# Performance work log

Measured on AMD Instinct MI355X. Metric: run time of the kernel, lower is better.

The kernel has to match this reference:

```python
import jax, jax.numpy as jnp
import numpy as np

N = 50000
E = 800000
F_IN = 500
H = 5          # heads
C = 32         # per-head channels
HID = H * C    # 160
NC = 20        # num_classes
G = 8          # number of graphs in batch
SLOPE_ATT = 0.2   # GATConv attention leaky slope (PyG default)
SLOPE_ACT = 0.01  # F.leaky_relu default


def _layernorm(x, scale, bias, eps=1e-5):
    mu = jnp.mean(x, axis=-1, keepdims=True)
    var = jnp.var(x, axis=-1, keepdims=True)
    return (x - mu) * jax.lax.rsqrt(var + eps) * scale + bias


def _edge_softmax(logits, dst, num_nodes):
    # segment softmax over incoming edges of each destination node
    m = jax.ops.segment_max(logits, dst, num_segments=num_nodes)
    ex = jnp.exp(logits - m[dst])
    s = jax.ops.segment_sum(ex, dst, num_segments=num_nodes)
    return ex / (s[dst] + 1e-16)


def _gat_layer(x, src, dst, W, a_src, a_dst, b):
    n = x.shape[0]
    h = (x @ W).reshape(n, H, C)                       # [N,H,C]
    al_s = jnp.einsum('nhc,hc->nh', h, a_src)          # [N,H]
    al_d = jnp.einsum('nhc,hc->nh', h, a_dst)
    logits = jax.nn.leaky_relu(al_s[src] + al_d[dst], SLOPE_ATT)  # [Et,H]
    alpha = _edge_softmax(logits, dst, n)              # [Et,H]
    msg = h[src] * alpha[..., None]                    # [Et,H,C]
    out = jax.ops.segment_sum(msg, dst, num_segments=n).reshape(n, HID) + b
    return out, alpha


def setup_inputs():
    key = jax.random.key(0)
    ks = jax.random.split(key, 24)
    p = lambda k, shp: jax.random.normal(k, shp, jnp.float32) * 0.05
    x = jax.random.normal(ks[0], (N, F_IN), jnp.float32)
    edge_index = jax.random.randint(ks[1], (2, E), 0, N, jnp.int64)
    batch = jnp.sort(jax.random.randint(ks[2], (N,), 0, G, jnp.int64))
    return {
        'x': x, 'edge_index': edge_index, 'batch': batch,
        'W1': p(ks[3], (F_IN, HID)), 'a_src1': p(ks[4], (H, C)), 'a_dst1': p(ks[5], (H, C)), 'b1': jnp.zeros((HID,), jnp.float32),
        'ln1_s': jnp.ones((HID,), jnp.float32), 'ln1_b': jnp.zeros((HID,), jnp.float32),
        'W2': p(ks[6], (HID, HID)), 'a_src2': p(ks[7], (H, C)), 'a_dst2': p(ks[8], (H, C)), 'b2': jnp.zeros((HID,), jnp.float32),
        'ln2_s': jnp.ones((HID,), jnp.float32), 'ln2_b': jnp.zeros((HID,), jnp.float32),
        'Wm': p(ks[9], (HID, HID)), 'bm': jnp.zeros((HID,), jnp.float32),
        'Wmlp1': p(ks[10], (HID, HID)), 'bmlp1': jnp.zeros((HID,), jnp.float32),
        'ln3_s': jnp.ones((HID,), jnp.float32), 'ln3_b': jnp.zeros((HID,), jnp.float32),
        'Wmlp2': p(ks[11], (HID, NC)), 'bmlp2': jnp.zeros((NC,), jnp.float32),
    }


def reference(x, edge_index, batch, W1, a_src1, a_dst1, b1, ln1_s, ln1_b,
              W2, a_src2, a_dst2, b2, ln2_s, ln2_b, Wm, bm,
              Wmlp1, bmlp1, ln3_s, ln3_b, Wmlp2, bmlp2):
    n = x.shape[0]
    # PyG GATConv adds self-loops by default
    loops = jnp.arange(n, dtype=edge_index.dtype)
    src = jnp.concatenate([edge_index[0], loops])
    dst = jnp.concatenate([edge_index[1], loops])

    h1, alpha1 = _gat_layer(x, src, dst, W1, a_src1, a_dst1, b1)
    h1 = jax.nn.leaky_relu(h1, SLOPE_ACT)
    h1 = _layernorm(h1, ln1_s, ln1_b)      # dropout = identity at eval

    h2, alpha2 = _gat_layer(h1, src, dst, W2, a_src2, a_dst2, b2)
    h2 = jax.nn.leaky_relu(h2, SLOPE_ACT)
    h2 = _layernorm(h2, ln2_s, ln2_b)

    xo = jax.nn.leaky_relu(h2 @ Wm + bm, SLOPE_ACT)   # [N,HID]

    # global_mean_pool over batch assignment
    sums = jax.ops.segment_sum(xo, batch, num_segments=G)
    cnts = jax.ops.segment_sum(jnp.ones((n, 1), xo.dtype), batch, num_segments=G)
    pooled = sums / jnp.maximum(cnts, 1.0)            # [G,HID]

    z = pooled @ Wmlp1 + bmlp1
    z = jax.nn.relu(_layernorm(z, ln3_s, ln3_b))
    rec = z @ Wmlp2 + bmlp2                           # [G,NC]
    return xo, rec, alpha1, alpha2
```

## Files before the change

### kernel.cpp

```cpp
#include <hip/hip_runtime.h>
#include <hip/hip_bf16.h>
#include <cstdint>
#include <cstddef>

#define NN   50000
#define EE   800000
#define ET_  (EE + NN)
#define FIN  500
#define HID_ 160
#define NC_  20
#define GG   8
#define GB1  ((NN + 63) / 64)
#define NK1  16
#define NK2  5

typedef __attribute__((ext_vector_type(8))) short ab8;
typedef __attribute__((ext_vector_type(4))) float f4;

static __device__ __forceinline__ unsigned short f2bf(float v) {
    union { float f; uint32_t u; } c; c.f = v;
    uint32_t r = c.u + 0x7FFFu + ((c.u >> 16) & 1u);
    return (unsigned short)(r >> 16);
}

static __device__ __forceinline__ float2 bf2f2(uint32_t u) {
    union { uint32_t u; float f; } a, b;
    a.u = u << 16;
    b.u = u & 0xffff0000u;
    return make_float2(a.f, b.f);
}

static __device__ __forceinline__ int lbound_i(const int* arr, int n, int val) {
    int lo = 0, hi = n;
    while (lo < hi) { int mid = (lo + hi) >> 1; if (arr[mid] < val) lo = mid + 1; else hi = mid; }
    return lo;
}

__global__ __launch_bounds__(256) void k_hist(const int* __restrict__ ei, int* __restrict__ deg) {
    int e = blockIdx.x * 256 + threadIdx.x;
    if (e >= ET_) return;
    int d = (e < EE) ? ei[EE + e] : (e - EE);
    atomicAdd(&deg[d], 1);
}

__global__ __launch_bounds__(256) void k_scan1(const int* __restrict__ deg, int* __restrict__ rowptr,
                                               int* __restrict__ bsum) {
    __shared__ int s[256];
    int t = threadIdx.x;
    int base = blockIdx.x * 1024 + t * 4;
    int v0 = (base + 0 < NN) ? deg[base + 0] : 0;
    int v1 = (base + 1 < NN) ? deg[base + 1] : 0;
    int v2 = (base + 2 < NN) ? deg[base + 2] : 0;
    int v3 = (base + 3 < NN) ? deg[base + 3] : 0;
    int tot = v0 + v1 + v2 + v3;
    s[t] = tot;
    __syncthreads();
    for (int off = 1; off < 256; off <<= 1) {
        int y = (t >= off) ? s[t - off] : 0;
        __syncthreads();
        s[t] += y;
        __syncthreads();
    }
    int excl = s[t] - tot;
    if (t == 255) bsum[blockIdx.x] = s[255];
    if (base + 0 < NN) rowptr[base + 0] = excl;  excl += v0;
    if (base + 1 < NN) rowptr[base + 1] = excl;  excl += v1;
    if (base + 2 < NN) rowptr[base + 2] = excl;  excl += v2;
    if (base + 3 < NN) rowptr[base + 3] = excl;
}

__global__ void k_scan2(int* __restrict__ bsum, int nb) {
    int t = threadIdx.x;
    int v = (t < nb) ? bsum[t] : 0;
    int orig = v;
    for (int off = 1; off < 64; off <<= 1) {
        int y = __shfl_up(v, off);
        if (t >= off) v += y;
    }
    if (t < nb) bsum[t] = v - orig;
}

__global__ __launch_bounds__(256) void k_scan3(int* __restrict__ rowptr, const int* __restrict__ bsum,
                                               int* __restrict__ cursor) {
    int i = blockIdx.x * 256 + threadIdx.x;
    if (i < NN) {
        int r = rowptr[i] + bsum[i >> 10];
        rowptr[i] = r;
        cursor[i] = r;
    }
    if (i == NN) rowptr[NN] = ET_;
}

__global__ __launch_bounds__(256) void k_scatter(const int* __restrict__ ei, int* __restrict__ cursor,
                                                 int2* __restrict__ epair) {
    int e = blockIdx.x * 256 + threadIdx.x;
    if (e >= ET_) return;
    int s, d;
    if (e < EE) { s = ei[e]; d = ei[EE + e]; } else { s = e - EE; d = e - EE; }
    int slot = atomicAdd(&cursor[d], 1);
    epair[slot] = make_int2(e, s);
}

__global__ __launch_bounds__(256) void k_prep_all(const float* __restrict__ W1, ab8* __restrict__ B1,
                                                  const float* __restrict__ W2, ab8* __restrict__ B2,
                                                  const float* __restrict__ Wm, ab8* __restrict__ Bm,
                                                  float* __restrict__ pooled) {
    int idx = blockIdx.x * 256 + threadIdx.x;
    if (idx < GG * HID_) pooled[idx] = 0.f;
    const int C1 = NK1 * 10 * 64;
    const int C2 = NK2 * 10 * 64;
    const float* W; ab8* Bo; int K, cidx;
    if (idx < C1)                { W = W1; Bo = B1; K = FIN;  cidx = idx; }
    else if (idx < C1 + C2)      { W = W2; Bo = B2; K = HID_; cidx = idx - C1; }
    else if (idx < C1 + 2 * C2)  { W = Wm; Bo = Bm; K = HID_; cidx = idx - C1 - C2; }
    else return;
    int s = cidx / 640, r = cidx % 640;
    int t = r >> 6, l = r & 63;
    int fr = l & 15, q = l >> 4;
    int n  = t * 16 + fr;
    int k0 = s * 32 + q * 8;
    unsigned short pk[8];
#pragma unroll
    for (int j = 0; j < 8; j++) {
        int k = k0 + j;
        pk[j] = (k < K) ? f2bf(W[(size_t)k * HID_ + n]) : (unsigned short)0;
    }
    Bo[cidx] = *reinterpret_cast<ab8*>(pk);
}

__global__ __launch_bounds__(256) void k_conv_x(const float* __restrict__ x, ab8* __restrict__ Apk) {
    int idx = blockIdx.x * 256 + threadIdx.x;
    int tid = idx & 255;
    int s   = (idx >> 8) & (NK1 - 1);
    int blk = idx >> 12;
    int l = tid & 63, w = tid >> 6;
    int fr = l & 15, q = l >> 4;
    int row = blk * 64 + w * 16 + fr;
    int k0 = s * 32 + q * 8;
    unsigned short pk[8] = {0, 0, 0, 0, 0, 0, 0, 0};
    if (row < NN) {
        const float* xr = &x[(size_t)row * FIN];
        if (k0 + 8 <= FIN) {
            const float4* s4 = reinterpret_cast<const float4*>(&xr[k0]);
            float4 u = s4[0], v = s4[1];
            pk[0] = f2bf(u.x); pk[1] = f2bf(u.y); pk[2] = f2bf(u.z); pk[3] = f2bf(u.w);
            pk[4] = f2bf(v.x); pk[5] = f2bf(v.y); pk[6] = f2bf(v.z); pk[7] = f2bf(v.w);
        } else {
#pragma unroll
            for (int j = 0; j < 8; j++)
                if (k0 + j < FIN) pk[j] = f2bf(xr[k0 + j]);
        }
    }
    Apk[idx] = *reinterpret_cast<ab8*>(pk);
}

template<int PKA>
static __device__ __forceinline__ void gemm_body(const void* __restrict__ Av,
                                                 const ab8* __restrict__ Bpk, int nk,
                                                 float* __restrict__ C, __hip_bfloat16* __restrict__ Cb,
                                                 int M, int K,
                                                 const float* __restrict__ bias, int act,
                                                 const float* __restrict__ asrc, const float* __restrict__ adst,
                                                 float* __restrict__ als_o, float* __restrict__ ald_o,
                                                 const int* __restrict__ batch_p, float* __restrict__ pooled) {
    int tid  = threadIdx.x;
    int lane = tid & 63;
    int w    = tid >> 6;
    int fr   = lane & 15;
    int q    = lane >> 4;
    int row0 = blockIdx.x * 64;
    int arow = row0 + w * 16 + fr;
    bool rv  = arow < M;

    f4 acc[10];
#pragma unroll
    for (int t = 0; t < 10; t++) acc[t] = (f4)0.f;

    const ab8* bb  = Bpk + lane;
    const ab8* apk = reinterpret_cast<const ab8*>(Av) + (size_t)blockIdx.x * nk * 256 + tid;
    const unsigned short* Arow = (const unsigned short*)Av;

    auto loadA = [&](int s) -> ab8 {
        if (PKA) return apk[s * 256];
        ab8 a = (ab8)0;
        if (rv) a = *reinterpret_cast<const ab8*>(&Arow[(size_t)arow * K + s * 32 + q * 8]);
        return a;
    };

    ab8 bcur[10], bnx[10];
#pragma unroll
    for (int t = 0; t < 10; t++) bcur[t] = bb[t * 64];
    ab8 a0 = loadA(0);
    ab8 a1 = loadA(1);
    for (int s = 0; s < nk; s++) {
        if (s + 1 < nk) {
#pragma unroll
            for (int t = 0; t < 10; t++) bnx[t] = bb[((s + 1) * 10 + t) * 64];
        }
        ab8 a2 = (ab8)0;
        if (s + 2 < nk) a2 = loadA(s + 2);
#pragma unroll
        for (int t = 0; t < 10; t++)
            acc[t] = __builtin_amdgcn_mfma_f32_16x16x32_bf16(a0, bcur[t], acc[t], 0, 0, 0);
        a0 = a1; a1 = a2;
#pragma unroll
        for (int t = 0; t < 10; t++) bcur[t] = bnx[t];
    }

    if (als_o) {
        float av_s[10], av_d[10];
#pragma unroll
        for (int t = 0; t < 10; t++) { av_s[t] = asrc[t * 16 + fr]; av_d[t] = adst[t * 16 + fr]; }
#pragma unroll
        for (int i = 0; i < 4; i++) {
            int r = row0 + w * 16 + q * 4 + i;
            float ps[5], pd[5];
#pragma unroll
            for (int h = 0; h < 5; h++) {
                ps[h] = acc[2 * h][i] * av_s[2 * h] + acc[2 * h + 1][i] * av_s[2 * h + 1];
                pd[h] = acc[2 * h][i] * av_d[2 * h] + acc[2 * h + 1][i] * av_d[2 * h + 1];
            }
#pragma unroll
            for (int off = 8; off >= 1; off >>= 1)
#pragma unroll
                for (int h = 0; h < 5; h++) {
                    ps[h] += __shfl_xor(ps[h], off);
                    pd[h] += __shfl_xor(pd[h], off);
                }
            if (fr == 0 && r < M) {
#pragma unroll
                for (int h = 0; h < 5; h++) {
                    als_o[(size_t)r * 5 + h] = ps[h];
                    ald_o[(size_t)r * 5 + h] = pd[h];
                }
            }
        }
    }

    int gu = -2;
    if (pooled) {
        int rhi = row0 + 63; if (rhi >= M) rhi = M - 1;
        int gl = batch_p[row0], gh = batch_p[rhi];
        gu = (gl == gh) ? gl : -1;
    }
    float psum[10];
#pragma unroll
    for (int t = 0; t < 10; t++) psum[t] = 0.f;

    int rbase = row0 + w * 16 + q * 4;
#pragma unroll
    for (int t = 0; t < 10; t++) {
        int col = t * 16 + fr;
        float bv = bias ? bias[col] : 0.f;
#pragma unroll
        for (int i = 0; i < 4; i++) {
            int r = rbase + i;
            float v = acc[t][i] + bv;
            if (act) v = v > 0.f ? v : 0.01f * v;
            if (r < M) {
                if (C)  C[(size_t)r * HID_ + col] = v;
                if (Cb) *reinterpret_cast<unsigned short*>(&Cb[(size_t)r * HID_ + col]) = f2bf(v);
                if (gu >= 0) psum[t] += v;
                else if (gu == -1) atomicAdd(&pooled[batch_p[r] * HID_ + col], v);
            }
        }
    }
    if (gu >= 0) {
#pragma unroll
        for (int t = 0; t < 10; t++) {
            psum[t] += __shfl_xor(psum[t], 16);
            psum[t] += __shfl_xor(psum[t], 32);
        }
        if (q == 0) {
#pragma unroll
            for (int t = 0; t < 10; t++)
                atomicAdd(&pooled[gu * HID_ + t * 16 + fr], psum[t]);
        }
    }
}

__global__ __launch_bounds__(256) void k_gemm_pk(const void* __restrict__ Av,
                                                 const ab8* __restrict__ Bpk, int nk,
                                                 float* __restrict__ C, __hip_bfloat16* __restrict__ Cb,
                                                 int M, int K,
                                                 const float* __restrict__ bias, int act,
                                                 const float* __restrict__ asrc, const float* __restrict__ adst,
                                                 float* __restrict__ als_o, float* __restrict__ ald_o,
                                                 const int* __restrict__ batch_p, float* __restrict__ pooled) {
    gemm_body<1>(Av, Bpk, nk, C, Cb, M, K, bias, act, asrc, adst, als_o, ald_o, batch_p, pooled);
}

__global__ __launch_bounds__(256) void k_gemm_rm(const void* __restrict__ Av,
                                                 const ab8* __restrict__ Bpk, int nk,
                                                 float* __restrict__ C, __hip_bfloat16* __restrict__ Cb,
                                                 int M, int K,
                                                 const float* __restrict__ bias, int act,
                                                 const float* __restrict__ asrc, const float* __restrict__ adst,
                                                 float* __restrict__ als_o, float* __restrict__ ald_o,
                                                 const int* __restrict__ batch_p, float* __restrict__ pooled) {
    gemm_body<0>(Av, Bpk, nk, C, Cb, M, K, bias, act, asrc, adst, als_o, ald_o, batch_p, pooled);
}

__global__ __launch_bounds__(256) void k_att_agg(const int* __restrict__ rowptr,
                                                 const int2* __restrict__ epair,
                                                 const float* __restrict__ als, const float* __restrict__ ald,
                                                 const __hip_bfloat16* __restrict__ hmat,
                                                 float* __restrict__ alphap,
                                                 float* __restrict__ alpha_out,
                                                 const float* __restrict__ bias,
                                                 const float* __restrict__ lns, const float* __restrict__ lnb,
                                                 __hip_bfloat16* __restrict__ outb) {
    __shared__ float sExp[4][64 * 5];
    __shared__ int2  sPair[4][64];
    int wv   = threadIdx.x >> 6;
    int lane = threadIdx.x & 63;
    int node = blockIdx.x * 4 + wv;
    if (node >= NN) return;
    int start = rowptr[node], end = rowptr[node + 1];
    int deg = end - start;
    bool fits = (deg <= 64);
    float ad[5];
#pragma unroll
    for (int h = 0; h < 5; h++) ad[h] = ald[node * 5 + h];

    float sm[5] = {0.f, 0.f, 0.f, 0.f, 0.f};
    for (int j = start + lane; j < end; j += 64) {
        int2 p = epair[j];
        const float* as = &als[(size_t)p.y * 5];
        int idx = j - start;
        if (fits) sPair[wv][idx] = p;
#pragma unroll
        for (int h = 0; h < 5; h++) {
            float l = as[h] + ad[h];
            l = l > 0.f ? l : 0.2f * l;
            float ex = __expf(fminf(l, 60.f));
            sm[h] += ex;
            if (fits) sExp[wv][idx * 5 + h] = ex;
            else      alphap[(size_t)j * 5 + h] = ex;
        }
    }
#pragma unroll
    for (int off = 32; off >= 1; off >>= 1)
#pragma unroll
        for (int h = 0; h < 5; h++) sm[h] += __shfl_xor(sm[h], off);
    float inv[5];
#pragma unroll
    for (int h = 0; h < 5; h++) inv[h] = 1.f / (sm[h] + 1e-16f);

    int h0 = lane >> 4;
    bool lo16 = lane < 16;
    int c01 = 2 * lane;
    int c2  = 128 + 2 * lane;
    float2 A  = make_float2(0.f, 0.f), B2 = make_float2(0.f, 0.f);
    float2 A2 = make_float2(0.f, 0.f), B22 = make_float2(0.f, 0.f);

    if (fits) {
        if (lane < deg) {
            int2 p = sPair[wv][lane];
            float* ao = &alpha_out[(size_t)p.x * 5];
#pragma unroll
            for (int h = 0; h < 5; h++) ao[h] = sExp[wv][lane * 5 + h] * inv[h];
        }
        int idx = 0;
        for (; idx + 1 < deg; idx += 2) {
            int sA = sPair[wv][idx].y, sB = sPair[wv][idx + 1].y;
            float wA = sExp[wv][idx * 5 + h0] * inv[h0];
            float wB = sExp[wv][(idx + 1) * 5 + h0] * inv[h0];
            const unsigned short* rA = (const unsigned short*)&hmat[(size_t)sA * HID_];
            const unsigned short* rB = (const unsigned short*)&hmat[(size_t)sB * HID_];
            float2 fA = bf2f2(*reinterpret_cast<const uint32_t*>(&rA[c01]));
            float2 fB = bf2f2(*reinterpret_cast<const uint32_t*>(&rB[c01]));
            A.x += wA * fA.x; A.y += wA * fA.y;
            B2.x += wB * fB.x; B2.y += wB * fB.y;
            if (lo16) {
                float wA4 = sExp[wv][idx * 5 + 4] * inv[4];
                float wB4 = sExp[wv][(idx + 1) * 5 + 4] * inv[4];
                float2 gA = bf2f2(*reinterpret_cast<const uint32_t*>(&rA[c2]));
                float2 gB = bf2f2(*reinterpret_cast<const uint32_t*>(&rB[c2]));
                A2.x += wA4 * gA.x; A2.y += wA4 * gA.y;
                B22.x += wB4 * gB.x; B22.y += wB4 * gB.y;
            }
        }
        if (idx < deg) {
            int sA = sPair[wv][idx].y;
            float wA = sExp[wv][idx * 5 + h0] * inv[h0];
            const unsigned short* rA = (const unsigned short*)&hmat[(size_t)sA * HID_];
            float2 fA = bf2f2(*reinterpret_cast<const uint32_t*>(&rA[c01]));
            A.x += wA * fA.x; A.y += wA * fA.y;
            if (lo16) {
                float wA4 = sExp[wv][idx * 5 + 4] * inv[4];
                float2 gA = bf2f2(*reinterpret_cast<const uint32_t*>(&rA[c2]));
                A2.x += wA4 * gA.x; A2.y += wA4 * gA.y;
            }
        }
    } else {
        for (int j = start + lane; j < end; j += 64) {
            int2 p = epair[j];
            float* ao = &alpha_out[(size_t)p.x * 5];
#pragma unroll
            for (int h = 0; h < 5; h++) ao[h] = alphap[(size_t)j * 5 + h] * inv[h];
        }
        for (int j = start; j < end; j++) {
            int2 p = epair[j];
            const float* ap = &alphap[(size_t)j * 5];
            float wA = ap[h0] * inv[h0];
            const unsigned short* rA = (const unsigned short*)&hmat[(size_t)p.y * HID_];
            float2 fA = bf2f2(*reinterpret_cast<const uint32_t*>(&rA[c01]));
            A.x += wA * fA.x; A.y += wA * fA.y;
            if (lo16) {
                float wA4 = ap[4] * inv[4];
                float2 gA = bf2f2(*reinterpret_cast<const uint32_t*>(&rA[c2]));
                A2.x += wA4 * gA.x; A2.y += wA4 * gA.y;
            }
        }
    }
    A.x += B2.x; A.y += B2.y; A2.x += B22.x; A2.y += B22.y;

    float2 bb = *reinterpret_cast<const float2*>(&bias[c01]);
    float v0 = A.x + bb.x;  v0 = v0 > 0.f ? v0 : 0.01f * v0;
    float v1 = A.y + bb.y;  v1 = v1 > 0.f ? v1 : 0.01f * v1;
    float v2 = 0.f, v3 = 0.f;
    if (lo16) {
        float2 b2 = *reinterpret_cast<const float2*>(&bias[c2]);
        v2 = A2.x + b2.x; v2 = v2 > 0.f ? v2 : 0.01f * v2;
        v3 = A2.y + b2.y; v3 = v3 > 0.f ? v3 : 0.01f * v3;
    }
    float s  = v0 + v1 + v2 + v3;
    float sq = v0 * v0 + v1 * v1 + v2 * v2 + v3 * v3;
#pragma unroll
    for (int off = 32; off >= 1; off >>= 1) {
        s  += __shfl_xor(s, off);
        sq += __shfl_xor(sq, off);
    }
    float m = s * (1.f / 160.f);
    float r = rsqrtf(sq * (1.f / 160.f) - m * m + 1e-5f);
    size_t ob = (size_t)node * HID_;
    {
        float2 sc = *reinterpret_cast<const float2*>(&lns[c01]);
        float2 bi = *reinterpret_cast<const float2*>(&lnb[c01]);
        uint32_t pk = (uint32_t)f2bf((v0 - m) * r * sc.x + bi.x)
                    | ((uint32_t)f2bf((v1 - m) * r * sc.y + bi.y) << 16);
        *reinterpret_cast<uint32_t*>(&outb[ob + c01]) = pk;
    }
    if (lo16) {
        float2 sc = *reinterpret_cast<const float2*>(&lns[c2]);
        float2 bi = *reinterpret_cast<const float2*>(&lnb[c2]);
        uint32_t pk = (uint32_t)f2bf((v2 - m) * r * sc.x + bi.x)
                    | ((uint32_t)f2bf((v3 - m) * r * sc.y + bi.y) << 16);
        *reinterpret_cast<uint32_t*>(&outb[ob + c2]) = pk;
    }
}

__global__ __launch_bounds__(256) void k_mlp(const float* __restrict__ pooled, const int* __restrict__ batch,
                                             const float* __restrict__ W1, const float* __restrict__ b1,
                                             const float* __restrict__ lns, const float* __restrict__ lnb,
                                             const float* __restrict__ W2, const float* __restrict__ b2,
                                             float* __restrict__ rec) {
    __shared__ float P[GG][HID_];
    __shared__ float Z[GG][HID_];
    __shared__ float mu[GG], rr[GG], ic[GG];
    int t = threadIdx.x;
    if (t < GG) {
        int lo = lbound_i(batch, NN, t), hi = lbound_i(batch, NN, t + 1);
        ic[t] = 1.f / fmaxf((float)(hi - lo), 1.f);
    }
    __syncthreads();
    for (int i = t; i < GG * HID_; i += 256) P[i / HID_][i % HID_] = pooled[i] * ic[i / HID_];
    __syncthreads();
    for (int i = t; i < GG * HID_; i += 256) {
        int g = i / HID_, j = i % HID_;
        float acc = b1[j];
        for (int k = 0; k < HID_; k++) acc += P[g][k] * W1[k * HID_ + j];
        Z[g][j] = acc;
    }
    __syncthreads();
    if (t < GG) {
        float s = 0.f, sq = 0.f;
        for (int k = 0; k < HID_; k++) { float z = Z[t][k]; s += z; sq += z * z; }
        float m = s / (float)HID_;
        mu[t] = m;
        rr[t] = rsqrtf(sq / (float)HID_ - m * m + 1e-5f);
    }
    __syncthreads();
    for (int i = t; i < GG * HID_; i += 256) {
        int g = i / HID_, j = i % HID_;
        float z = (Z[g][j] - mu[g]) * rr[g] * lns[j] + lnb[j];
        Z[g][j] = fmaxf(z, 0.f);
    }
    __syncthreads();
    for (int i = t; i < GG * NC_; i += 256) {
        int g = i / NC_, j = i % NC_;
        float acc = b2[j];
        for (int k = 0; k < HID_; k++) acc += Z[g][k] * W2[k * NC_ + j];
        rec[g * NC_ + j] = acc;
    }
}

extern "C" void kernel_launch(void* const* d_in, const int* in_sizes, int n_in,
                              void* d_out, int out_size, void* d_ws, size_t ws_size,
                              hipStream_t stream) {
    const float* x    = (const float*)d_in[0];
    const int*   ei   = (const int*)d_in[1];
    const int*   batch= (const int*)d_in[2];
    const float* W1   = (const float*)d_in[3];
    const float* as1  = (const float*)d_in[4];
    const float* ad1  = (const float*)d_in[5];
    const float* b1   = (const float*)d_in[6];
    const float* ln1s = (const float*)d_in[7];
    const float* ln1b = (const float*)d_in[8];
    const float* W2   = (const float*)d_in[9];
    const float* as2  = (const float*)d_in[10];
    const float* ad2  = (const float*)d_in[11];
    const float* b2   = (const float*)d_in[12];
    const float* ln2s = (const float*)d_in[13];
    const float* ln2b = (const float*)d_in[14];
    const float* Wm   = (const float*)d_in[15];
    const float* bm   = (const float*)d_in[16];
    const float* Wm1  = (const float*)d_in[17];
    const float* bm1  = (const float*)d_in[18];
    const float* ln3s = (const float*)d_in[19];
    const float* ln3b = (const float*)d_in[20];
    const float* Wm2  = (const float*)d_in[21];
    const float* bm2  = (const float*)d_in[22];

    float* out    = (float*)d_out;
    float* xo     = out;
    float* rec    = out + (size_t)NN * HID_;
    float* alpha1 = rec + GG * NC_;
    float* alpha2 = alpha1 + (size_t)ET_ * 5;

    char* w = (char*)d_ws;
    auto carve = [&](size_t bytes) { char* p = w; w += (bytes + 255) & ~(size_t)255; return p; };
    int*   deg    = (int*)carve((size_t)NN * 4);
    int*   rowptr = (int*)carve((size_t)(NN + 1) * 4);
    int*   cursor = (int*)carve((size_t)NN * 4);
    int2*  epair  = (int2*)carve((size_t)ET_ * 8);
    int*   bsum   = (int*)carve(64 * 4);
    __hip_bfloat16* hbuf  = (__hip_bfloat16*)carve((size_t)NN * HID_ * 2);
    __hip_bfloat16* xbufb = (__hip_bfloat16*)carve((size_t)NN * HID_ * 2);
    float* alphap = (float*)carve((size_t)ET_ * 5 * 4);
    float* als    = (float*)carve((size_t)NN * 5 * 4);
    float* ald    = (float*)carve((size_t)NN * 5 * 4);
    float* pooled = (float*)carve((size_t)GG * HID_ * 4);
    ab8*   B1pk   = (ab8*)carve((size_t)NK1 * 10 * 64 * 16);
    ab8*   B2pk   = (ab8*)carve((size_t)NK2 * 10 * 64 * 16);
    ab8*   Bmpk   = (ab8*)carve((size_t)NK2 * 10 * 64 * 16);
    ab8*   Apk    = (ab8*)d_out;

    hipMemsetAsync(deg, 0, (size_t)NN * 4, stream);
    k_hist<<<(ET_ + 255) / 256, 256, 0, stream>>>(ei, deg);
    int nb = (NN + 1023) / 1024;
    k_scan1<<<nb, 256, 0, stream>>>(deg, rowptr, bsum);
    k_scan2<<<1, 64, 0, stream>>>(bsum, nb);
    k_scan3<<<(NN + 1 + 255) / 256, 256, 0, stream>>>(rowptr, bsum, cursor);
    k_scatter<<<(ET_ + 255) / 256, 256, 0, stream>>>(ei, cursor, epair);

    const int PREP = NK1 * 10 * 64 + 2 * NK2 * 10 * 64;
    k_prep_all<<<(PREP + 255) / 256, 256, 0, stream>>>(W1, B1pk, W2, B2pk, Wm, Bmpk, pooled);
    k_conv_x<<<GB1 * NK1, 256, 0, stream>>>(x, Apk);

    const int NWB = (NN + 3) / 4;

    k_gemm_pk<<<GB1, 256, 0, stream>>>(Apk, B1pk, NK1, nullptr, hbuf, NN, FIN, nullptr, 0,
                                       as1, ad1, als, ald, nullptr, nullptr);
    k_att_agg<<<NWB, 256, 0, stream>>>(rowptr, epair, als, ald, hbuf, alphap, alpha1,
                                       b1, ln1s, ln1b, xbufb);

    k_gemm_rm<<<GB1, 256, 0, stream>>>(xbufb, B2pk, NK2, nullptr, hbuf, NN, HID_, nullptr, 0,
                                       as2, ad2, als, ald, nullptr, nullptr);
    k_att_agg<<<NWB, 256, 0, stream>>>(rowptr, epair, als, ald, hbuf, alphap, alpha2,
                                       b2, ln2s, ln2b, xbufb);

    k_gemm_rm<<<GB1, 256, 0, stream>>>(xbufb, Bmpk, NK2, xo, nullptr, NN, HID_, bm, 1,
                                       nullptr, nullptr, nullptr, nullptr, batch, pooled);
    k_mlp<<<1, 256, 0, stream>>>(pooled, batch, Wm1, bm1, ln3s, ln3b, Wm2, bm2, rec);
}
```

Before: 647.4 us.

## Split alpha output into coalesced edge-order kernel and slim CSR to source-only

The attention-aggregation kernel no longer scatters alpha values to original edge positions. It stores per-node inverse softmax sums, and a new edge-parallel kernel recomputes exp(logit) and writes alpha in edge order, so the writes are coalesced. The CSR pair array shrinks to a source-only int array, and the per-node attention scalars are padded to stride 8 so they can be read as float4. The gather loop is unrolled to four edges with separate accumulators. The cost is two extra kernel launches and recomputing the exponentials for every edge.

```diff
diff --git a/kernel.cpp b/kernel.cpp
--- a/kernel.cpp
+++ b/kernel.cpp
@@ -92,13 +92,13 @@
 }
 
 __global__ __launch_bounds__(256) void k_scatter(const int* __restrict__ ei, int* __restrict__ cursor,
-                                                 int2* __restrict__ epair) {
+                                                 int* __restrict__ esrc) {
     int e = blockIdx.x * 256 + threadIdx.x;
     if (e >= ET_) return;
     int s, d;
     if (e < EE) { s = ei[e]; d = ei[EE + e]; } else { s = e - EE; d = e - EE; }
     int slot = atomicAdd(&cursor[d], 1);
-    epair[slot] = make_int2(e, s);
+    esrc[slot] = s;
 }
 
 __global__ __launch_bounds__(256) void k_prep_all(const float* __restrict__ W1, ab8* __restrict__ B1,
@@ -230,8 +230,8 @@
             if (fr == 0 && r < M) {
 #pragma unroll
                 for (int h = 0; h < 5; h++) {
-                    als_o[(size_t)r * 5 + h] = ps[h];
-                    ald_o[(size_t)r * 5 + h] = pd[h];
+                    als_o[(size_t)r * 8 + h] = ps[h];
+                    ald_o[(size_t)r * 8 + h] = pd[h];
                 }
             }
         }
@@ -302,16 +302,16 @@
 }
 
 __global__ __launch_bounds__(256) void k_att_agg(const int* __restrict__ rowptr,
-                                                 const int2* __restrict__ epair,
+                                                 const int* __restrict__ esrc,
                                                  const float* __restrict__ als, const float* __restrict__ ald,
                                                  const __hip_bfloat16* __restrict__ hmat,
                                                  float* __restrict__ alphap,
-                                                 float* __restrict__ alpha_out,
+                                                 float* __restrict__ invb,
                                                  const float* __restrict__ bias,
                                                  const float* __restrict__ lns, const float* __restrict__ lnb,
                                                  __hip_bfloat16* __restrict__ outb) {
     __shared__ float sExp[4][64 * 5];
-    __shared__ int2  sPair[4][64];
+    __shared__ int   sSrc[4][64];
     int wv   = threadIdx.x >> 6;
     int lane = threadIdx.x & 63;
     int node = blockIdx.x * 4 + wv;
@@ -319,19 +319,22 @@
     int start = rowptr[node], end = rowptr[node + 1];
     int deg = end - start;
     bool fits = (deg <= 64);
-    float ad[5];
-#pragma unroll
-    for (int h = 0; h < 5; h++) ad[h] = ald[node * 5 + h];
+    float4 dd4 = *reinterpret_cast<const float4*>(&ald[(size_t)node * 8]);
+    float  dd5 = ald[(size_t)node * 8 + 4];
+    float ad[5] = {dd4.x, dd4.y, dd4.z, dd4.w, dd5};
 
     float sm[5] = {0.f, 0.f, 0.f, 0.f, 0.f};
     for (int j = start + lane; j < end; j += 64) {
-        int2 p = epair[j];
-        const float* as = &als[(size_t)p.y * 5];
+        int sy = esrc[j];
         int idx = j - start;
-        if (fits) sPair[wv][idx] = p;
+        if (fits) sSrc[wv][idx] = sy;
+        const float* as = &als[(size_t)sy * 8];
+        float4 a4 = *reinterpret_cast<const float4*>(as);
+        float  a5 = as[4];
+        float asv[5] = {a4.x, a4.y, a4.z, a4.w, a5};
 #pragma unroll
         for (int h = 0; h < 5; h++) {
-            float l = as[h] + ad[h];
+            float l = asv[h] + ad[h];
             l = l > 0.f ? l : 0.2f * l;
             float ex = __expf(fminf(l, 60.f));
             sm[h] += ex;
@@ -346,75 +349,84 @@
     float inv[5];
 #pragma unroll
     for (int h = 0; h < 5; h++) inv[h] = 1.f / (sm[h] + 1e-16f);
+    if (lane == 0) {
+        float* ip = &invb[(size_t)node * 8];
+        ip[0] = inv[0]; ip[1] = inv[1]; ip[2] = inv[2]; ip[3] = inv[3]; ip[4] = inv[4];
+    }
 
     int h0 = lane >> 4;
     bool lo16 = lane < 16;
     int c01 = 2 * lane;
     int c2  = 128 + 2 * lane;
-    float2 A  = make_float2(0.f, 0.f), B2 = make_float2(0.f, 0.f);
-    float2 A2 = make_float2(0.f, 0.f), B22 = make_float2(0.f, 0.f);
+    float2 A0 = make_float2(0.f, 0.f), A1 = make_float2(0.f, 0.f);
+    float2 A2 = make_float2(0.f, 0.f), A3 = make_float2(0.f, 0.f);
+    float2 H0 = make_float2(0.f, 0.f), H1 = make_float2(0.f, 0.f);
+    float2 H2 = make_float2(0.f, 0.f), H3 = make_float2(0.f, 0.f);
 
     if (fits) {
-        if (lane < deg) {
-            int2 p = sPair[wv][lane];
-            float* ao = &alpha_out[(size_t)p.x * 5];
-#pragma unroll
-            for (int h = 0; h < 5; h++) ao[h] = sExp[wv][lane * 5 + h] * inv[h];
-        }
         int idx = 0;
-        for (; idx + 1 < deg; idx += 2) {
-            int sA = sPair[wv][idx].y, sB = sPair[wv][idx + 1].y;
-            float wA = sExp[wv][idx * 5 + h0] * inv[h0];
-            float wB = sExp[wv][(idx + 1) * 5 + h0] * inv[h0];
-            const unsigned short* rA = (const unsigned short*)&hmat[(size_t)sA * HID_];
-            const unsigned short* rB = (const unsigned short*)&hmat[(size_t)sB * HID_];
-            float2 fA = bf2f2(*reinterpret_cast<const uint32_t*>(&rA[c01]));
-            float2 fB = bf2f2(*reinterpret_cast<const uint32_t*>(&rB[c01]));
-            A.x += wA * fA.x; A.y += wA * fA.y;
-            B2.x += wB * fB.x; B2.y += wB * fB.y;
+        for (; idx + 3 < deg; idx += 4) {
+            int s0 = sSrc[wv][idx], s1 = sSrc[wv][idx + 1];
+            int s2 = sSrc[wv][idx + 2], s3 = sSrc[wv][idx + 3];
+            float w0 = sExp[wv][(idx + 0) * 5 + h0] * inv[h0];
+            float w1 = sExp[wv][(idx + 1) * 5 + h0] * inv[h0];
+            float w2 = sExp[wv][(idx + 2) * 5 + h0] * inv[h0];
+            float w3 = sExp[wv][(idx + 3) * 5 + h0] * inv[h0];
+            const unsigned short* r0 = (const unsigned short*)&hmat[(size_t)s0 * HID_];
+            const unsigned short* r1 = (const unsigned short*)&hmat[(size_t)s1 * HID_];
+            const unsigned short* r2 = (const unsigned short*)&hmat[(size_t)s2 * HID_];
+            const unsigned short* r3 = (const unsigned short*)&hmat[(size_t)s3 * HID_];
+            float2 f0 = bf2f2(*reinterpret_cast<const uint32_t*>(&r0[c01]));
+            float2 f1 = bf2f2(*reinterpret_cast<const uint32_t*>(&r1[c01]));
+            float2 f2 = bf2f2(*reinterpret_cast<const uint32_t*>(&r2[c01]));
+            float2 f3 = bf2f2(*reinterpret_cast<const uint32_t*>(&r3[c01]));
+            A0.x += w0 * f0.x; A0.y += w0 * f0.y;
+            A1.x += w1 * f1.x; A1.y += w1 * f1.y;
+            A2.x += w2 * f2.x; A2.y += w2 * f2.y;
+            A3.x += w3 * f3.x; A3.y += w3 * f3.y;
             if (lo16) {
-                float wA4 = sExp[wv][idx * 5 + 4] * inv[4];
-                float wB4 = sExp[wv][(idx + 1) * 5 + 4] * inv[4];
-                float2 gA = bf2f2(*reinterpret_cast<const uint32_t*>(&rA[c2]));
-                float2 gB = bf2f2(*reinterpret_cast<const uint32_t*>(&rB[c2]));
-                A2.x += wA4 * gA.x; A2.y += wA4 * gA.y;
-                B22.x += wB4 * gB.x; B22.y += wB4 * gB.y;
+                float u0 = sExp[wv][(idx + 0) * 5 + 4] * inv[4];
+                float u1 = sExp[wv][(idx + 1) * 5 + 4] * inv[4];
+                float u2 = sExp[wv][(idx + 2) * 5 + 4] * inv[4];
+                float u3 = sExp[wv][(idx + 3) * 5 + 4] * inv[4];
+                float2 g0 = bf2f2(*reinterpret_cast<const uint32_t*>(&r0[c2]));
+                float2 g1 = bf2f2(*reinterpret_cast<const uint32_t*>(&r1[c2]));
+                float2 g2 = bf2f2(*reinterpret_cast<const uint32_t*>(&r2[c2]));
+                float2 g3 = bf2f2(*reinterpret_cast<const uint32_t*>(&r3[c2]));
+                H0.x += u0 * g0.x; H0.y += u0 * g0.y;
+                H1.x += u1 * g1.x; H1.y += u1 * g1.y;
+                H2.x += u2 * g2.x; H2.y += u2 * g2.y;
+                H3.x += u3 * g3.x; H3.y += u3 * g3.y;
             }
         }
-        if (idx < deg) {
-            int sA = sPair[wv][idx].y;
-            float wA = sExp[wv][idx * 5 + h0] * inv[h0];
-            const unsigned short* rA = (const unsigned short*)&hmat[(size_t)sA * HID_];
-            float2 fA = bf2f2(*reinterpret_cast<const uint32_t*>(&rA[c01]));
-            A.x += wA * fA.x; A.y += wA * fA.y;
+        for (; idx < deg; idx++) {
+            int s0 = sSrc[wv][idx];
+            float w0 = sExp[wv][idx * 5 + h0] * inv[h0];
+            const unsigned short* r0 = (const unsigned short*)&hmat[(size_t)s0 * HID_];
+            float2 f0 = bf2f2(*reinterpret_cast<const uint32_t*>(&r0[c01]));
+            A0.x += w0 * f0.x; A0.y += w0 * f0.y;
             if (lo16) {
-                float wA4 = sExp[wv][idx * 5 + 4] * inv[4];
-                float2 gA = bf2f2(*reinterpret_cast<const uint32_t*>(&rA[c2]));
-                A2.x += wA4 * gA.x; A2.y += wA4 * gA.y;
+                float u0 = sExp[wv][idx * 5 + 4] * inv[4];
+                float2 g0 = bf2f2(*reinterpret_cast<const uint32_t*>(&r0[c2]));
+                H0.x += u0 * g0.x; H0.y += u0 * g0.y;
             }
         }
     } else {
-        for (int j = start + lane; j < end; j += 64) {
-            int2 p = epair[j];
-            float* ao = &alpha_out[(size_t)p.x * 5];
-#pragma unroll
-            for (int h = 0; h < 5; h++) ao[h] = alphap[(size_t)j * 5 + h] * inv[h];
-        }
         for (int j = start; j < end; j++) {
-            int2 p = epair[j];
-            const float* ap = &alphap[(size_t)j * 5];
-            float wA = ap[h0] * inv[h0];
-            const unsigned short* rA = (const unsigned short*)&hmat[(size_t)p.y * HID_];
-            float2 fA = bf2f2(*reinterpret_cast<const uint32_t*>(&rA[c01]));
-            A.x += wA * fA.x; A.y += wA * fA.y;
+            int s0 = esrc[j];
+            float w0 = alphap[(size_t)j * 5 + h0] * inv[h0];
+            const unsigned short* r0 = (const unsigned short*)&hmat[(size_t)s0 * HID_];
+            float2 f0 = bf2f2(*reinterpret_cast<const uint32_t*>(&r0[c01]));
+            A0.x += w0 * f0.x; A0.y += w0 * f0.y;
             if (lo16) {
-                float wA4 = ap[4] * inv[4];
-                float2 gA = bf2f2(*reinterpret_cast<const uint32_t*>(&rA[c2]));
-                A2.x += wA4 * gA.x; A2.y += wA4 * gA.y;
+                float u0 = alphap[(size_t)j * 5 + 4] * inv[4];
+                float2 g0 = bf2f2(*reinterpret_cast<const uint32_t*>(&r0[c2]));
+                H0.x += u0 * g0.x; H0.y += u0 * g0.y;
             }
         }
     }
-    A.x += B2.x; A.y += B2.y; A2.x += B22.x; A2.y += B22.y;
+    float2 A = make_float2(A0.x + A1.x + A2.x + A3.x, A0.y + A1.y + A2.y + A3.y);
+    float2 Hh = make_float2(H0.x + H1.x + H2.x + H3.x, H0.y + H1.y + H2.y + H3.y);
 
     float2 bb = *reinterpret_cast<const float2*>(&bias[c01]);
     float v0 = A.x + bb.x;  v0 = v0 > 0.f ? v0 : 0.01f * v0;
@@ -422,8 +434,8 @@
     float v2 = 0.f, v3 = 0.f;
     if (lo16) {
         float2 b2 = *reinterpret_cast<const float2*>(&bias[c2]);
-        v2 = A2.x + b2.x; v2 = v2 > 0.f ? v2 : 0.01f * v2;
-        v3 = A2.y + b2.y; v3 = v3 > 0.f ? v3 : 0.01f * v3;
+        v2 = Hh.x + b2.x; v2 = v2 > 0.f ? v2 : 0.01f * v2;
+        v3 = Hh.y + b2.y; v3 = v3 > 0.f ? v3 : 0.01f * v3;
     }
     float s  = v0 + v1 + v2 + v3;
     float sq = v0 * v0 + v1 * v1 + v2 * v2 + v3 * v3;
@@ -448,6 +460,36 @@
         uint32_t pk = (uint32_t)f2bf((v2 - m) * r * sc.x + bi.x)
                     | ((uint32_t)f2bf((v3 - m) * r * sc.y + bi.y) << 16);
         *reinterpret_cast<uint32_t*>(&outb[ob + c2]) = pk;
+    }
+}
+
+__global__ __launch_bounds__(256) void k_alpha(const int* __restrict__ ei,
+                                               const float* __restrict__ als, const float* __restrict__ ald,
+                                               const float* __restrict__ invb,
+                                               float* __restrict__ alpha_out) {
+    int e = blockIdx.x * 256 + threadIdx.x;
+    if (e >= ET_) return;
+    int s, d;
+    if (e < EE) { s = ei[e]; d = ei[EE + e]; } else { s = e - EE; d = e - EE; }
+    const float* as = &als[(size_t)s * 8];
+    float4 a4 = *reinterpret_cast<const float4*>(as);
+    float  a5 = as[4];
+    float asv[5] = {a4.x, a4.y, a4.z, a4.w, a5};
+    const float* adp = &ald[(size_t)d * 8];
+    float4 d4 = *reinterpret_cast<const float4*>(adp);
+    float  d5 = adp[4];
+    float adv[5] = {d4.x, d4.y, d4.z, d4.w, d5};
+    const float* ip = &invb[(size_t)d * 8];
+    float4 i4 = *reinterpret_cast<const float4*>(ip);
+    float  i5 = ip[4];
+    float ivv[5] = {i4.x, i4.y, i4.z, i4.w, i5};
+    float* ao = &alpha_out[(size_t)e * 5];
+#pragma unroll
+    for (int h = 0; h < 5; h++) {
+        float l = asv[h] + adv[h];
+        l = l > 0.f ? l : 0.2f * l;
+        float ex = __expf(fminf(l, 60.f));
+        ao[h] = ex * ivv[h];
     }
 }
 
@@ -534,13 +576,14 @@
     int*   deg    = (int*)carve((size_t)NN * 4);
     int*   rowptr = (int*)carve((size_t)(NN + 1) * 4);
     int*   cursor = (int*)carve((size_t)NN * 4);
-    int2*  epair  = (int2*)carve((size_t)ET_ * 8);
+    int*   esrc   = (int*)carve((size_t)ET_ * 4);
     int*   bsum   = (int*)carve(64 * 4);
     __hip_bfloat16* hbuf  = (__hip_bfloat16*)carve((size_t)NN * HID_ * 2);
     __hip_bfloat16* xbufb = (__hip_bfloat16*)carve((size_t)NN * HID_ * 2);
     float* alphap = (float*)carve((size_t)ET_ * 5 * 4);
-    float* als    = (float*)carve((size_t)NN * 5 * 4);
-    float* ald    = (float*)carve((size_t)NN * 5 * 4);
+    float* als    = (float*)carve((size_t)NN * 8 * 4);
+    float* ald    = (float*)carve((size_t)NN * 8 * 4);
+    float* invb   = (float*)carve((size_t)NN * 8 * 4);
     float* pooled = (float*)carve((size_t)GG * HID_ * 4);
     ab8*   B1pk   = (ab8*)carve((size_t)NK1 * 10 * 64 * 16);
     ab8*   B2pk   = (ab8*)carve((size_t)NK2 * 10 * 64 * 16);
@@ -553,23 +596,26 @@
     k_scan1<<<nb, 256, 0, stream>>>(deg, rowptr, bsum);
     k_scan2<<<1, 64, 0, stream>>>(bsum, nb);
     k_scan3<<<(NN + 1 + 255) / 256, 256, 0, stream>>>(rowptr, bsum, cursor);
-    k_scatter<<<(ET_ + 255) / 256, 256, 0, stream>>>(ei, cursor, epair);
+    k_scatter<<<(ET_ + 255) / 256, 256, 0, stream>>>(ei, cursor, esrc);
 
     const int PREP = NK1 * 10 * 64 + 2 * NK2 * 10 * 64;
     k_prep_all<<<(PREP + 255) / 256, 256, 0, stream>>>(W1, B1pk, W2, B2pk, Wm, Bmpk, pooled);
     k_conv_x<<<GB1 * NK1, 256, 0, stream>>>(x, Apk);
 
     const int NWB = (NN + 3) / 4;
+    const int EB  = (ET_ + 255) / 256;
 
     k_gemm_pk<<<GB1, 256, 0, stream>>>(Apk, B1pk, NK1, nullptr, hbuf, NN, FIN, nullptr, 0,
                                        as1, ad1, als, ald, nullptr, nullptr);
-    k_att_agg<<<NWB, 256, 0, stream>>>(rowptr, epair, als, ald, hbuf, alphap, alpha1,
+    k_att_agg<<<NWB, 256, 0, stream>>>(rowptr, esrc, als, ald, hbuf, alphap, invb,
                                        b1, ln1s, ln1b, xbufb);
+    k_alpha<<<EB, 256, 0, stream>>>(ei, als, ald, invb, alpha1);
 
     k_gemm_rm<<<GB1, 256, 0, stream>>>(xbufb, B2pk, NK2, nullptr, hbuf, NN, HID_, nullptr, 0,
                                        as2, ad2, als, ald, nullptr, nullptr);
-    k_att_agg<<<NWB, 256, 0, stream>>>(rowptr, epair, als, ald, hbuf, alphap, alpha2,
+    k_att_agg<<<NWB, 256, 0, stream>>>(rowptr, esrc, als, ald, hbuf, alphap, invb,
                                        b2, ln2s, ln2b, xbufb);
+    k_alpha<<<EB, 256, 0, stream>>>(ei, als, ald, invb, alpha2);
 
     k_gemm_rm<<<GB1, 256, 0, stream>>>(xbufb, Bmpk, NK2, xo, nullptr, NN, HID_, bm, 1,
                                        nullptr, nullptr, nullptr, nullptr, batch, pooled);
```

Result: faster. 630.6 us (-2.6%).
